# Kernel optimization log

Measured on AMD Instinct MI355X. Metric: run time of the kernel, lower is better.

## Reference

```python
import jax, jax.numpy as jnp
import numpy as np

NUM_HEADS = 12
HEAD_DIM = 64
EPS = 1e-6


def _layernorm(x, g, b):
    mu = jnp.mean(x, axis=-1, keepdims=True)
    var = jnp.mean(jnp.square(x - mu), axis=-1, keepdims=True)
    return (x - mu) * jax.lax.rsqrt(var + EPS) * g + b


def setup_inputs() -> dict:
    key = jax.random.key(0)
    ks = jax.random.split(key, 8)
    D, DFF = 768, 3072
    s = lambda d: 1.0 / np.sqrt(d)
    return {
        "hidden_states": jax.random.normal(ks[0], (4, 2048, D), jnp.float32),
        "ln1_g": jnp.ones((D,), jnp.float32),
        "ln1_b": jnp.zeros((D,), jnp.float32),
        "w_qkv": jax.random.normal(ks[1], (D, 3 * D), jnp.float32) * s(D),
        "b_qkv": jnp.zeros((3 * D,), jnp.float32),
        "w_attn": jax.random.normal(ks[2], (D, D), jnp.float32) * s(D),
        "b_attn": jnp.zeros((D,), jnp.float32),
        "ln2_g": jnp.ones((D,), jnp.float32),
        "ln2_b": jnp.zeros((D,), jnp.float32),
        "w_in": jax.random.normal(ks[3], (D, DFF), jnp.float32) * s(D),
        "b_in": jnp.zeros((DFF,), jnp.float32),
        "w_out": jax.random.normal(ks[4], (DFF, D), jnp.float32) * s(DFF),
        "b_out": jnp.zeros((D,), jnp.float32),
    }


def reference(hidden_states, ln1_g, ln1_b, w_qkv, b_qkv, w_attn, b_attn,
              ln2_g, ln2_b, w_in, b_in, w_out, b_out):
    B, S, D = hidden_states.shape
    residual = hidden_states
    h = _layernorm(hidden_states, ln1_g, ln1_b)
    # QKV: [B,S,3D] -> [B,S,3,H,hd] -> [3,B,H,S,hd]
    qkv = (h @ w_qkv + b_qkv).reshape(B, S, 3, NUM_HEADS, HEAD_DIM)
    qkv = jnp.transpose(qkv, (2, 0, 3, 1, 4))
    scale = HEAD_DIM ** (-0.5)
    q, k, v = qkv[0] * scale, qkv[1], qkv[2]
    scores = jnp.einsum("bhqd,bhkd->bhqk", q, k)
    attn = jax.nn.softmax(scores, axis=-1)
    o = jnp.einsum("bhqk,bhkd->bhqd", attn, v)
    o = jnp.transpose(o, (0, 2, 1, 3)).reshape(B, S, D)
    h = residual + (o @ w_attn + b_attn)
    residual2 = h
    h2 = _layernorm(h, ln2_g, ln2_b)
    h2 = jax.nn.gelu(h2 @ w_in + b_in, approximate=False)
    h2 = h2 @ w_out + b_out
    return residual2 + h2
```

## Files before the change

kernel.cpp:

```cpp
#include <hip/hip_runtime.h>

typedef __bf16 bf16_t;
typedef bf16_t bf16x8 __attribute__((ext_vector_type(8)));
typedef float f32x4 __attribute__((ext_vector_type(4)));
typedef unsigned short ushortx8 __attribute__((ext_vector_type(8)));
typedef unsigned short ushortx4 __attribute__((ext_vector_type(4)));
typedef short short4v __attribute__((ext_vector_type(4)));

union UB8 { bf16_t h8[8]; bf16x8 b; };

__device__ __forceinline__ unsigned short f2bf(float f) {
  union { bf16_t h; unsigned short u; } cv;
  cv.h = (bf16_t)f;
  return cv.u;
}

__device__ __forceinline__ void gl_lds16(const unsigned short* g, unsigned short* l) {
  __builtin_amdgcn_global_load_lds((const __attribute__((address_space(1))) void*)g,
                                   (__attribute__((address_space(3))) void*)l,
                                   16, 0, 0);
}

__device__ __forceinline__ float gelu_fast(float v) {
  float v3 = v * v * v;
  float z = -2.30211886f * v - 0.102945f * v3;
  float e = exp2f(z);
  return v * __builtin_amdgcn_rcpf(1.0f + e);
}

__global__ __launch_bounds__(256) void ln_kernel(const float* __restrict__ x,
                                                 const float* __restrict__ g,
                                                 const float* __restrict__ b,
                                                 unsigned short* __restrict__ out) {
  int row = blockIdx.x;
  int t = threadIdx.x;
  const float* xr = x + (size_t)row * 768;
  float v0 = xr[t], v1 = xr[t + 256], v2 = xr[t + 512];
  __shared__ float red[4];
  float s = v0 + v1 + v2;
  for (int o = 32; o > 0; o >>= 1) s += __shfl_down(s, o, 64);
  if ((t & 63) == 0) red[t >> 6] = s;
  __syncthreads();
  float mu = (red[0] + red[1] + red[2] + red[3]) * (1.0f / 768.0f);
  __syncthreads();
  float d0 = v0 - mu, d1 = v1 - mu, d2 = v2 - mu;
  s = d0 * d0 + d1 * d1 + d2 * d2;
  for (int o = 32; o > 0; o >>= 1) s += __shfl_down(s, o, 64);
  if ((t & 63) == 0) red[t >> 6] = s;
  __syncthreads();
  float var = (red[0] + red[1] + red[2] + red[3]) * (1.0f / 768.0f);
  float rs = rsqrtf(var + 1e-6f);
  unsigned short* orow = out + (size_t)row * 768;
  orow[t]       = f2bf(d0 * rs * g[t]       + b[t]);
  orow[t + 256] = f2bf(d1 * rs * g[t + 256] + b[t + 256]);
  orow[t + 512] = f2bf(d2 * rs * g[t + 512] + b[t + 512]);
}

__global__ __launch_bounds__(256) void transpose_all(
    const float* __restrict__ w_qkv, const float* __restrict__ w_attn,
    const float* __restrict__ w_in, const float* __restrict__ w_out,
    unsigned short* __restrict__ wqkvT, unsigned short* __restrict__ wattnT,
    unsigned short* __restrict__ winT, unsigned short* __restrict__ woutT) {
  int id = blockIdx.x;
  const float* W; unsigned short* WT; int K, N, nx, ny;
  if (id < 1728)      { W = w_qkv;  WT = wqkvT;  K = 768;  N = 2304; nx = id % 72; ny = id / 72; }
  else if (id < 2304) { id -= 1728; W = w_attn; WT = wattnT; K = 768;  N = 768;  nx = id % 24; ny = id / 24; }
  else if (id < 4608) { id -= 2304; W = w_in;   WT = winT;   K = 768;  N = 3072; nx = id % 96; ny = id / 96; }
  else                { id -= 4608; W = w_out;  WT = woutT;  K = 3072; N = 768;  nx = id % 24; ny = id / 24; }
  __shared__ float tile[32][33];
  int n0 = nx * 32, k0 = ny * 32;
  int tx = threadIdx.x, ty = threadIdx.y;
  for (int i = 0; i < 4; i++)
    tile[ty + i * 8][tx] = W[(size_t)(k0 + ty + i * 8) * N + n0 + tx];
  __syncthreads();
  for (int i = 0; i < 4; i++)
    WT[(size_t)(n0 + ty + i * 8) * K + k0 + tx] = f2bf(tile[tx][ty + i * 8]);
}

template <int EPI, int TM>
__device__ __forceinline__ void gemm_body(const unsigned short* __restrict__ A,
                                          const unsigned short* __restrict__ BT,
                                          const float* __restrict__ bias,
                                          const float* resid,
                                          void* out, unsigned short* vt, int os,
                                          int N, int K) {
  constexpr int BK = 32, MI = TM / 32;
  constexpr int ASZ = TM * BK;
  constexpr int BUF = ASZ + 128 * BK;
  __shared__ __align__(16) unsigned short smem[3 * BUF];

  int t = threadIdx.x;
  int w = t >> 6, lane = t & 63, ln = lane & 15, quad = lane >> 4;
  int wm = w & 1, wn = w >> 1;

  int gx = gridDim.x;
  int nwg = gx * gridDim.y;
  int flat = blockIdx.y * gx + blockIdx.x;
  int nf = (flat & 7) * (nwg >> 3) + (flat >> 3);
  int m0 = (nf / gx) * TM, n0 = (nf % gx) * 128;

  int Kc = (EPI == 3) ? (K / (int)gridDim.z) : K;
  int kbase = (EPI == 3) ? ((int)blockIdx.z * Kc) : 0;

  int lrow = lane >> 2;
  int lslot = lane & 3;
  int scol = (lslot ^ ((lrow >> 1) & 3)) * 8;

  const unsigned short* gA0 = A + (size_t)(m0 + w * 16 + lrow) * K + kbase + scol;
  const unsigned short* gA1 = gA0 + (size_t)64 * K;
  const unsigned short* gB0 = BT + (size_t)(n0 + w * 16 + lrow) * K + kbase + scol;
  const unsigned short* gB1 = gB0 + (size_t)64 * K;

  auto stage = [&](int buf) {
    unsigned short* Sb = smem + buf * BUF;
    gl_lds16(gA0, Sb + w * 512);
    if constexpr (TM == 128) { gl_lds16(gA1, Sb + 2048 + w * 512); gA1 += BK; }
    gl_lds16(gB0, Sb + ASZ + w * 512);
    gl_lds16(gB1, Sb + ASZ + 2048 + w * 512);
    gA0 += BK; gB0 += BK; gB1 += BK;
  };

  f32x4 acc[MI][4];
  f32x4 zero = {0.f, 0.f, 0.f, 0.f};
  for (int mi = 0; mi < MI; mi++)
    for (int ni = 0; ni < 4; ni++) acc[mi][ni] = zero;

  int nk = Kc / BK;
  stage(0);
  stage(1);
  int cur = 0;
  int soff = (quad ^ ((ln >> 1) & 3)) * 8;
  for (int kt = 0; kt < nk; kt++) {
    if (kt < nk - 1) {
      if constexpr (TM == 128) asm volatile("s_waitcnt vmcnt(4)" ::: "memory");
      else                     asm volatile("s_waitcnt vmcnt(3)" ::: "memory");
    } else {
      asm volatile("s_waitcnt vmcnt(0)" ::: "memory");
    }
    __builtin_amdgcn_s_barrier();
    __builtin_amdgcn_sched_barrier(0);
    int pre = cur + 2; if (pre >= 3) pre -= 3;
    if (kt + 2 < nk) stage(pre);
    const unsigned short* Sc = smem + cur * BUF;
    bf16x8 af[MI], bfr[4];
#pragma unroll
    for (int mi = 0; mi < MI; mi++)
      af[mi] = *(const bf16x8*)&Sc[(wm * (TM / 2) + mi * 16 + ln) * 32 + soff];
#pragma unroll
    for (int ni = 0; ni < 4; ni++)
      bfr[ni] = *(const bf16x8*)&Sc[ASZ + (wn * 64 + ni * 16 + ln) * 32 + soff];
#pragma unroll
    for (int mi = 0; mi < MI; mi++)
#pragma unroll
      for (int ni = 0; ni < 4; ni++)
        acc[mi][ni] = __builtin_amdgcn_mfma_f32_16x16x32_bf16(af[mi], bfr[ni],
                                                              acc[mi][ni], 0, 0, 0);
    cur = cur + 1; if (cur >= 3) cur = 0;
  }

  if (EPI == 3) {
    float* outp = (float*)out;
    bool addb = (blockIdx.z == 0);
    for (int mi = 0; mi < MI; mi++) {
      for (int ni = 0; ni < 4; ni++) {
        int col = n0 + wn * 64 + ni * 16 + ln;
        float bv = addb ? bias[col] : 0.0f;
        for (int r = 0; r < 4; r++) {
          int row = m0 + wm * (TM / 2) + mi * 16 + quad * 4 + r;
          atomicAdd(&outp[(size_t)row * N + col], acc[mi][ni][r] + bv);
        }
      }
    }
  } else if (EPI == 2) {
    float* outp = (float*)out;
    for (int mi = 0; mi < MI; mi++) {
      for (int ni = 0; ni < 4; ni++) {
        int col = n0 + wn * 64 + ni * 16 + ln;
        float bv = bias[col];
        for (int r = 0; r < 4; r++) {
          int row = m0 + wm * (TM / 2) + mi * 16 + quad * 4 + r;
          float v = acc[mi][ni][r] + bv;
          v += resid[(size_t)row * N + col];
          outp[(size_t)row * N + col] = v;
        }
      }
    }
  } else {
    __syncthreads();
    unsigned short* Cs16 = smem + w * 1024;
    unsigned short* outp = (unsigned short*)out;
    for (int mi = 0; mi < MI; mi++) {
      for (int ni = 0; ni < 4; ni++) {
        int col = n0 + wn * 64 + ni * 16 + ln;
        float bv = bias[col];
        for (int r = 0; r < 4; r++) {
          float v = acc[mi][ni][r] + bv;
          if (EPI == 0) {
            if (col < 768) v *= 0.18033688f;
          } else {
            v = gelu_fast(v);
          }
          Cs16[(quad * 4 + r) * 64 + ni * 16 + ln] = f2bf(v);
        }
      }
      __syncthreads();
      if (EPI == 0 && n0 >= 1536) {
        int c = n0 - 1536 + wn * 64 + lane;
        int s0 = m0 + wm * (TM / 2) + mi * 16;
        int bb = s0 >> 11, sl = s0 & 2047;
        ushortx8 lo, hi;
        for (int r = 0; r < 8; r++) lo[r] = Cs16[r * 64 + lane];
        for (int r = 0; r < 8; r++) hi[r] = Cs16[(8 + r) * 64 + lane];
        size_t vbase = ((size_t)(bb * 768 + c)) * 2048 + sl;
        *(ushortx8*)&vt[vbase] = lo;
        *(ushortx8*)&vt[vbase + 8] = hi;
      } else {
        int OS = (EPI == 0) ? os : N;
        for (int j = 0; j < 2; j++) {
          int rrow = j * 8 + (lane >> 3);
          int ch = (lane & 7) * 8;
          ushortx8 pv = *(const ushortx8*)&Cs16[rrow * 64 + ch];
          *(ushortx8*)&outp[(size_t)(m0 + wm * (TM / 2) + mi * 16 + rrow) * OS +
                            n0 + wn * 64 + ch] = pv;
        }
      }
      __syncthreads();
    }
  }
}

__global__ __launch_bounds__(256) void gemm_qkv(const unsigned short* A,
    const unsigned short* BT, const float* bias, void* out, unsigned short* vt,
    int N, int K) {
  gemm_body<0, 128>(A, BT, bias, nullptr, out, vt, 1536, N, K);
}
__global__ __launch_bounds__(256) void gemm_attnout(const unsigned short* A,
    const unsigned short* BT, const float* bias, const float* resid, void* out,
    int N, int K) {
  gemm_body<2, 64>(A, BT, bias, resid, out, nullptr, N, N, K);
}
__global__ __launch_bounds__(256) void gemm_ffn1(const unsigned short* A,
    const unsigned short* BT, const float* bias, void* out, int N, int K) {
  gemm_body<1, 128>(A, BT, bias, nullptr, out, nullptr, N, N, K);
}
__global__ __launch_bounds__(256) void gemm_ffn2(const unsigned short* A,
    const unsigned short* BT, const float* bias, const float* resid, void* out,
    int N, int K) {
  gemm_body<3, 128>(A, BT, bias, resid, out, nullptr, N, N, K);
}

__global__ __launch_bounds__(512, 4) void flash_attn(
    const unsigned short* __restrict__ qk, const unsigned short* __restrict__ v_t,
    unsigned short* __restrict__ o) {
  int flat = blockIdx.y * 16 + blockIdx.x;
  int nf = (flat & 7) * 96 + (flat >> 3);
  int qt = nf % 16;
  int bh = nf / 16;
  int b = bh / 12, h = bh % 12;
  int t = threadIdx.x;
  int w = t >> 6, lane = t & 63, ln = lane & 15, quad = lane >> 4;
  int qg = w & 3, kh2 = w >> 2;

  __shared__ __align__(16) unsigned short smem[18432];
  int qrow0 = b * 2048 + qt * 128;
  int qw = qrow0 + qg * 32;

  bf16x8 qf[2][2];
  for (int qi = 0; qi < 2; qi++)
    for (int kh = 0; kh < 2; kh++)
      qf[qi][kh] = *(const bf16x8*)&qk[(size_t)(qw + qi * 16 + ln) * 1536 +
                                      h * 64 + kh * 32 + quad * 8];

  UB8 ones8;
#pragma unroll
  for (int r = 0; r < 8; r++) ones8.h8[r] = (bf16_t)1.0f;

  f32x4 zero = {0.f, 0.f, 0.f, 0.f};
  f32x4 o_acc[4][2];
  for (int df = 0; df < 4; df++)
    for (int qi = 0; qi < 2; qi++) o_acc[df][qi] = zero;
  f32x4 l_acc[2] = {zero, zero};

  int sr = t >> 3, sc = (t & 7) * 8;
  int ssr = (sr & 32) | (((sr >> 2) & 1) << 4) | (((sr >> 3) & 3) << 2) | (sr & 3);
  ushortx8 kreg = *(const ushortx8*)&qk[(size_t)(b * 2048 + sr) * 1536 + 768 + h * 64 + sc];
  ushortx8 vreg = *(const ushortx8*)&v_t[(size_t)(bh * 64 + sr) * 2048 + sc];

  for (int kt = 0; kt < 32; kt++) {
    unsigned short* Ks = smem + (kt & 1) * 9216;
    unsigned short* Vt = Ks + 4608;
    *(ushortx8*)&Ks[ssr * 72 + sc] = kreg;
    *(ushortx8*)&Vt[sr * 72 + sc] = vreg;
    __syncthreads();
    if (kt < 31) {
      int krow0 = b * 2048 + (kt + 1) * 64;
      kreg = *(const ushortx8*)&qk[(size_t)(krow0 + sr) * 1536 + 768 + h * 64 + sc];
      vreg = *(const ushortx8*)&v_t[(size_t)(bh * 64 + sr) * 2048 + (kt + 1) * 64 + sc];
    }

    UB8 pb[2];
#pragma unroll
    for (int kf = 0; kf < 2; kf++) {
      int krow = kh2 * 32 + kf * 16;
      f32x4 ST[2] = {zero, zero};
      bf16x8 kA0 = *(const bf16x8*)&Ks[(krow + ln) * 72 + quad * 8];
      bf16x8 kA1 = *(const bf16x8*)&Ks[(krow + ln) * 72 + 32 + quad * 8];
      __builtin_amdgcn_s_setprio(1);
#pragma unroll
      for (int qi = 0; qi < 2; qi++) {
        ST[qi] = __builtin_amdgcn_mfma_f32_16x16x32_bf16(kA0, qf[qi][0], ST[qi], 0, 0, 0);
        ST[qi] = __builtin_amdgcn_mfma_f32_16x16x32_bf16(kA1, qf[qi][1], ST[qi], 0, 0, 0);
      }
      __builtin_amdgcn_s_setprio(0);
#pragma unroll
      for (int qi = 0; qi < 2; qi++)
#pragma unroll
        for (int r = 0; r < 4; r++)
          pb[qi].h8[kf * 4 + r] = (bf16_t)__builtin_amdgcn_exp2f(ST[qi][r]);
    }
    __builtin_amdgcn_s_setprio(1);
#pragma unroll
    for (int qi = 0; qi < 2; qi++)
      l_acc[qi] = __builtin_amdgcn_mfma_f32_16x16x32_bf16(ones8.b, pb[qi].b,
                                                          l_acc[qi], 0, 0, 0);
#pragma unroll
    for (int df = 0; df < 4; df++) {
      bf16x8 vA = *(const bf16x8*)&Vt[(df * 16 + ln) * 72 + kh2 * 32 + quad * 8];
#pragma unroll
      for (int qi = 0; qi < 2; qi++)
        o_acc[df][qi] = __builtin_amdgcn_mfma_f32_16x16x32_bf16(vA, pb[qi].b,
                                                                o_acc[df][qi], 0, 0, 0);
    }
    __builtin_amdgcn_s_setprio(0);
  }

  __syncthreads();
  float* fb = (float*)smem;
  float* fbl = fb + 8320;
  if (kh2 == 1) {
    for (int df = 0; df < 4; df++)
      for (int qi = 0; qi < 2; qi++)
        for (int r = 0; r < 4; r++)
          fb[qg * 2080 + (qi * 16 + ln) * 65 + df * 16 + quad * 4 + r] =
              o_acc[df][qi][r];
    if (quad == 0)
      for (int qi = 0; qi < 2; qi++)
        fbl[qg * 32 + qi * 16 + ln] = l_acc[qi][0];
  }
  __syncthreads();
  float inv[2];
  if (kh2 == 0) {
    for (int qi = 0; qi < 2; qi++) {
      float lt = l_acc[qi][0] + fbl[qg * 32 + qi * 16 + ln];
      inv[qi] = __builtin_amdgcn_rcpf(lt);
    }
    for (int df = 0; df < 4; df++)
      for (int qi = 0; qi < 2; qi++)
        for (int r = 0; r < 4; r++)
          o_acc[df][qi][r] += fb[qg * 2080 + (qi * 16 + ln) * 65 + df * 16 + quad * 4 + r];
  }
  __syncthreads();
  if (kh2 == 0) {
    unsigned short* Osm = smem + qg * 2304;
    for (int qi = 0; qi < 2; qi++)
      for (int df = 0; df < 4; df++)
        for (int r = 0; r < 4; r++)
          Osm[(qi * 16 + ln) * 72 + df * 16 + quad * 4 + r] =
              f2bf(o_acc[df][qi][r] * inv[qi]);
  }
  __syncthreads();
  if (kh2 == 0) {
    unsigned short* Osm = smem + qg * 2304;
    for (int p2 = 0; p2 < 4; p2++) {
      int rr = p2 * 8 + (lane >> 3);
      int ch = (lane & 7) * 8;
      ushortx8 u = *(const ushortx8*)&Osm[rr * 72 + ch];
      *(ushortx8*)&o[(size_t)(qw + rr) * 768 + h * 64 + ch] = u;
    }
  }
}

extern "C" void kernel_launch(void* const* d_in, const int* in_sizes, int n_in,
                              void* d_out, int out_size, void* d_ws, size_t ws_size,
                              hipStream_t stream) {
  const float* hidden = (const float*)d_in[0];
  const float* ln1_g  = (const float*)d_in[1];
  const float* ln1_b  = (const float*)d_in[2];
  const float* w_qkv  = (const float*)d_in[3];
  const float* b_qkv  = (const float*)d_in[4];
  const float* w_attn = (const float*)d_in[5];
  const float* b_attn = (const float*)d_in[6];
  const float* ln2_g  = (const float*)d_in[7];
  const float* ln2_b  = (const float*)d_in[8];
  const float* w_in   = (const float*)d_in[9];
  const float* b_in   = (const float*)d_in[10];
  const float* w_out  = (const float*)d_in[11];
  const float* b_out  = (const float*)d_in[12];
  float* out = (float*)d_out;

  char* ws = (char*)d_ws;
  unsigned short* wqkvT  = (unsigned short*)(ws + 0);
  unsigned short* wattnT = (unsigned short*)(ws + 3538944);
  unsigned short* winT   = (unsigned short*)(ws + 4718592);
  unsigned short* woutT  = (unsigned short*)(ws + 9437184);
  unsigned short* bufX   = (unsigned short*)(ws + 14155776);
  unsigned short* bufBig = (unsigned short*)(ws + 26738688);
  unsigned short* bufQK  = bufBig;
  unsigned short* v_t    = (unsigned short*)(ws + 26738688 + 25165824);

  transpose_all<<<6912, dim3(32, 8), 0, stream>>>(w_qkv, w_attn, w_in, w_out,
                                                  wqkvT, wattnT, winT, woutT);
  ln_kernel<<<8192, 256, 0, stream>>>(hidden, ln1_g, ln1_b, bufX);
  gemm_qkv<<<dim3(18, 64), 256, 0, stream>>>(bufX, wqkvT, b_qkv, (void*)bufQK,
                                             v_t, 2304, 768);
  flash_attn<<<dim3(16, 48), 512, 0, stream>>>(bufQK, v_t, bufX);
  gemm_attnout<<<dim3(6, 128), 256, 0, stream>>>(bufX, wattnT, b_attn, hidden,
                                                 (void*)out, 768, 768);
  ln_kernel<<<8192, 256, 0, stream>>>(out, ln2_g, ln2_b, bufX);
  gemm_ffn1<<<dim3(24, 64), 256, 0, stream>>>(bufX, winT, b_in, (void*)bufBig,
                                              3072, 768);
  gemm_ffn2<<<dim3(6, 64, 2), 256, 0, stream>>>(bufBig, woutT, b_out, nullptr,
                                                (void*)out, 768, 3072);
}
```

Measured before the change: 373.3 us.

## Load B operand directly to registers and drop split-K atomics in FFN2

The GEMM body now keeps only the A tile in LDS, using a triple buffer. The B fragments are loaded straight from global memory into registers, double-buffered across an unrolled pair of k-steps. This frees LDS and removes the shared-memory reads for B, and the wait counts are adjusted to match. FFN2 no longer uses split-K with atomicAdd. It runs a single K pass and adds bias and residual in the epilogue, reading the residual from the output buffer in place. The trade-offs are fewer FFN2 workgroups, more scattered global loads for B, and a k-loop unrolled by two that assumes an even number of k-tiles.

```diff
diff --git a/kernel.cpp b/kernel.cpp
--- a/kernel.cpp
+++ b/kernel.cpp
@@ -86,8 +86,7 @@
                                           int N, int K) {
   constexpr int BK = 32, MI = TM / 32;
   constexpr int ASZ = TM * BK;
-  constexpr int BUF = ASZ + 128 * BK;
-  __shared__ __align__(16) unsigned short smem[3 * BUF];
+  __shared__ __align__(16) unsigned short smem[3 * ASZ];
 
   int t = threadIdx.x;
   int w = t >> 6, lane = t & 63, ln = lane & 15, quad = lane >> 4;
@@ -99,25 +98,32 @@
   int nf = (flat & 7) * (nwg >> 3) + (flat >> 3);
   int m0 = (nf / gx) * TM, n0 = (nf % gx) * 128;
 
-  int Kc = (EPI == 3) ? (K / (int)gridDim.z) : K;
-  int kbase = (EPI == 3) ? ((int)blockIdx.z * Kc) : 0;
-
   int lrow = lane >> 2;
   int lslot = lane & 3;
   int scol = (lslot ^ ((lrow >> 1) & 3)) * 8;
 
-  const unsigned short* gA0 = A + (size_t)(m0 + w * 16 + lrow) * K + kbase + scol;
+  const unsigned short* gA0 = A + (size_t)(m0 + w * 16 + lrow) * K + scol;
   const unsigned short* gA1 = gA0 + (size_t)64 * K;
-  const unsigned short* gB0 = BT + (size_t)(n0 + w * 16 + lrow) * K + kbase + scol;
-  const unsigned short* gB1 = gB0 + (size_t)64 * K;
 
   auto stage = [&](int buf) {
-    unsigned short* Sb = smem + buf * BUF;
+    unsigned short* Sb = smem + buf * ASZ;
     gl_lds16(gA0, Sb + w * 512);
+    gA0 += BK;
     if constexpr (TM == 128) { gl_lds16(gA1, Sb + 2048 + w * 512); gA1 += BK; }
-    gl_lds16(gB0, Sb + ASZ + w * 512);
-    gl_lds16(gB1, Sb + ASZ + 2048 + w * 512);
-    gA0 += BK; gB0 += BK; gB1 += BK;
+  };
+
+  const unsigned short* gB[4];
+#pragma unroll
+  for (int ni = 0; ni < 4; ni++)
+    gB[ni] = BT + (size_t)(n0 + wn * 64 + ni * 16 + ln) * K + quad * 8;
+
+  bf16x8 bE[4], bO[4];
+  auto loadB = [&](bf16x8* dst) {
+#pragma unroll
+    for (int ni = 0; ni < 4; ni++) {
+      dst[ni] = *(const bf16x8*)gB[ni];
+      gB[ni] += BK;
+    }
   };
 
   f32x4 acc[MI][4];
@@ -125,53 +131,45 @@
   for (int mi = 0; mi < MI; mi++)
     for (int ni = 0; ni < 4; ni++) acc[mi][ni] = zero;
 
-  int nk = Kc / BK;
-  stage(0);
-  stage(1);
+  int nk = K / BK;
   int cur = 0;
   int soff = (quad ^ ((ln >> 1) & 3)) * 8;
-  for (int kt = 0; kt < nk; kt++) {
+
+  auto kstep = [&](bf16x8* curB, bf16x8* nxtB, int kt) {
     if (kt < nk - 1) {
-      if constexpr (TM == 128) asm volatile("s_waitcnt vmcnt(4)" ::: "memory");
-      else                     asm volatile("s_waitcnt vmcnt(3)" ::: "memory");
+      if constexpr (TM == 128) asm volatile("s_waitcnt vmcnt(6)" ::: "memory");
+      else                     asm volatile("s_waitcnt vmcnt(5)" ::: "memory");
     } else {
       asm volatile("s_waitcnt vmcnt(0)" ::: "memory");
     }
     __builtin_amdgcn_s_barrier();
     __builtin_amdgcn_sched_barrier(0);
+    if (kt + 1 < nk) loadB(nxtB);
     int pre = cur + 2; if (pre >= 3) pre -= 3;
     if (kt + 2 < nk) stage(pre);
-    const unsigned short* Sc = smem + cur * BUF;
-    bf16x8 af[MI], bfr[4];
+    const unsigned short* Sc = smem + cur * ASZ;
+    bf16x8 af[MI];
 #pragma unroll
     for (int mi = 0; mi < MI; mi++)
       af[mi] = *(const bf16x8*)&Sc[(wm * (TM / 2) + mi * 16 + ln) * 32 + soff];
 #pragma unroll
-    for (int ni = 0; ni < 4; ni++)
-      bfr[ni] = *(const bf16x8*)&Sc[ASZ + (wn * 64 + ni * 16 + ln) * 32 + soff];
-#pragma unroll
     for (int mi = 0; mi < MI; mi++)
 #pragma unroll
       for (int ni = 0; ni < 4; ni++)
-        acc[mi][ni] = __builtin_amdgcn_mfma_f32_16x16x32_bf16(af[mi], bfr[ni],
+        acc[mi][ni] = __builtin_amdgcn_mfma_f32_16x16x32_bf16(af[mi], curB[ni],
                                                               acc[mi][ni], 0, 0, 0);
     cur = cur + 1; if (cur >= 3) cur = 0;
-  }
-
-  if (EPI == 3) {
-    float* outp = (float*)out;
-    bool addb = (blockIdx.z == 0);
-    for (int mi = 0; mi < MI; mi++) {
-      for (int ni = 0; ni < 4; ni++) {
-        int col = n0 + wn * 64 + ni * 16 + ln;
-        float bv = addb ? bias[col] : 0.0f;
-        for (int r = 0; r < 4; r++) {
-          int row = m0 + wm * (TM / 2) + mi * 16 + quad * 4 + r;
-          atomicAdd(&outp[(size_t)row * N + col], acc[mi][ni][r] + bv);
-        }
-      }
-    }
-  } else if (EPI == 2) {
+  };
+
+  stage(0);
+  loadB(bE);
+  stage(1);
+  for (int kt = 0; kt < nk; kt += 2) {
+    kstep(bE, bO, kt);
+    kstep(bO, bE, kt + 1);
+  }
+
+  if (EPI == 2) {
     float* outp = (float*)out;
     for (int mi = 0; mi < MI; mi++) {
       for (int ni = 0; ni < 4; ni++) {
@@ -246,7 +244,7 @@
 __global__ __launch_bounds__(256) void gemm_ffn2(const unsigned short* A,
     const unsigned short* BT, const float* bias, const float* resid, void* out,
     int N, int K) {
-  gemm_body<3, 128>(A, BT, bias, resid, out, nullptr, N, N, K);
+  gemm_body<2, 128>(A, BT, bias, resid, out, nullptr, N, N, K);
 }
 
 __global__ __launch_bounds__(512, 4) void flash_attn(
@@ -419,6 +417,6 @@
   ln_kernel<<<8192, 256, 0, stream>>>(out, ln2_g, ln2_b, bufX);
   gemm_ffn1<<<dim3(24, 64), 256, 0, stream>>>(bufX, winT, b_in, (void*)bufBig,
                                               3072, 768);
-  gemm_ffn2<<<dim3(6, 64, 2), 256, 0, stream>>>(bufBig, woutT, b_out, nullptr,
-                                                (void*)out, 768, 3072);
-}
+  gemm_ffn2<<<dim3(6, 64), 256, 0, stream>>>(bufBig, woutT, b_out, out,
+                                             (void*)out, 768, 3072);
+}
```

New measurement: 511.6 us. +37.0%, slower.
